# Optimization experiments

Hardware: AMD Instinct MI355X
Metric: run time of the kernel (lower is better)

Reference implementation:

```python
import jax, jax.numpy as jnp
import numpy as np

N = 16384   # nodes at current level
M = 8192    # nodes at next (coarser) level
E = 524288  # edges (avg degree 32)
D = 128     # in_feats == out_feats
LN_EPS = 1e-5


def setup_inputs() -> dict:
    key = jax.random.key(0)
    ks = jax.random.split(key, 10)
    curr_h = jax.random.normal(ks[0], (N, D), jnp.float32)
    next_h = jax.random.normal(ks[1], (M, D), jnp.float32)
    curr_inc = jax.random.uniform(ks[2], (N, M), jnp.float32)
    edge_src = jax.random.randint(ks[3], (E,), 0, N, jnp.int32)
    edge_dst = jax.random.randint(ks[4], (E,), 0, N, jnp.int32)
    Wc = jax.random.normal(ks[5], (D, D), jnp.float32) / np.float32(np.sqrt(D))
    Wf = jax.random.normal(ks[6], (D, D), jnp.float32) / np.float32(np.sqrt(D))
    bc = jnp.zeros((D,), jnp.float32)
    bf = jnp.zeros((D,), jnp.float32)
    conv_w = jax.random.uniform(ks[7], (D,), jnp.float32)
    topDown_w = jax.random.uniform(ks[8], (D,), jnp.float32)
    gamma = jnp.ones((D,), jnp.float32)
    beta = jnp.zeros((D,), jnp.float32)
    return dict(curr_h=curr_h, next_h=next_h, curr_inc=curr_inc,
                Wc=Wc, bc=bc, Wf=Wf, bf=bf, conv_w=conv_w,
                topDown_w=topDown_w, gamma=gamma, beta=beta,
                edge_src=edge_src, edge_dst=edge_dst)


def _graph_conv(x, W, b, src, dst, n):
    # DGL GraphConv, norm='both', on graph with self-loops added.
    ones = jnp.ones(src.shape[0], x.dtype)
    out_deg = jax.ops.segment_sum(ones, src, num_segments=n) + 1.0  # +1 self-loop
    in_deg = jax.ops.segment_sum(ones, dst, num_segments=n) + 1.0
    xn = x * jax.lax.rsqrt(out_deg)[:, None]
    # neighbor SpMM + self-loop contribution
    agg = jax.ops.segment_sum(xn[src], dst, num_segments=n) + xn
    agg = agg * jax.lax.rsqrt(in_deg)[:, None]
    return agg @ W + b


def reference(curr_h, next_h, curr_inc, Wc, bc, Wf, bf, conv_w,
              topDown_w, gamma, beta, edge_src, edge_dst):
    n = curr_h.shape[0]
    conv_layer = _graph_conv(curr_h, Wc, bc, edge_src, edge_dst, n) * conv_w[None, :]
    fused_in = curr_inc @ next_h  # dense incidence matmul [N, D]
    top_down = _graph_conv(fused_in, Wf, bf, edge_src, edge_dst, n) * topDown_w[None, :]
    res = (conv_layer + top_down) * 0.5  # update == 'MEAN' over stack of 2
    # LayerNorm over feature dim
    mu = jnp.mean(res, axis=-1, keepdims=True)
    var = jnp.mean(jnp.square(res - mu), axis=-1, keepdims=True)
    res = (res - mu) * jax.lax.rsqrt(var + LN_EPS) * gamma + beta
    res = jax.nn.relu(res)  # activation == 'RELU'
    # dropout: eval mode -> identity
    return res
```

## Files before the change

### kernel.cpp

```cpp
#include <hip/hip_runtime.h>

constexpr int Nn = 16384;
constexpr int Mm = 8192;
constexpr int Ee = 524288;
constexpr int Dd = 128;

typedef __attribute__((ext_vector_type(8))) short short8v;
typedef __attribute__((ext_vector_type(4))) short short4v;
typedef __attribute__((ext_vector_type(4))) float float4v;

static __device__ __forceinline__ short f2bf(float f) {
    unsigned u = __builtin_bit_cast(unsigned, f);
    u += 0x7fffu + ((u >> 16) & 1u);
    return (short)(u >> 16);
}

__global__ void k_zero_i(int* __restrict__ p, int n) {
    int i = blockIdx.x * 256 + threadIdx.x;
    if (i < n) p[i] = 0;
}

__global__ void k_deg_count(const int* __restrict__ src, const int* __restrict__ dst,
                            int* __restrict__ cnt_out, int* __restrict__ cnt_in) {
    int e = blockIdx.x * 256 + threadIdx.x;
    if (e < Ee) {
        atomicAdd(&cnt_out[src[e]], 1);
        atomicAdd(&cnt_in[dst[e]], 1);
    }
}

__global__ void k_deg_fin(const int* __restrict__ cnt_out, const int* __restrict__ cnt_in,
                          float* __restrict__ rs_out, float* __restrict__ rs_in) {
    int i = blockIdx.x * 256 + threadIdx.x;
    if (i < Nn) {
        rs_out[i] = rsqrtf((float)(cnt_out[i] + 1));
        rs_in[i]  = rsqrtf((float)(cnt_in[i] + 1));
    }
}

__global__ void k_scan(const int* __restrict__ cnt, int* __restrict__ row_start) {
    __shared__ int s[1024];
    int t = threadIdx.x;
    int base = t * 16;
    int local[16];
    int sum = 0;
#pragma unroll
    for (int i = 0; i < 16; i++) { local[i] = cnt[base + i]; sum += local[i]; }
    s[t] = sum;
    __syncthreads();
    for (int off = 1; off < 1024; off <<= 1) {
        int v = (t >= off) ? s[t - off] : 0;
        __syncthreads();
        s[t] += v;
        __syncthreads();
    }
    int run = s[t] - sum;
#pragma unroll
    for (int i = 0; i < 16; i++) { row_start[base + i] = run; run += local[i]; }
    if (t == 1023) row_start[16384] = s[1023];
}

__global__ void k_fill(const int* __restrict__ src, const int* __restrict__ dst,
                       const int* __restrict__ row_start, int* __restrict__ cursor,
                       int* __restrict__ ebuf) {
    int e = blockIdx.x * 256 + threadIdx.x;
    if (e < Ee) {
        int d = dst[e];
        int pos = atomicAdd(&cursor[d], 1);
        ebuf[row_start[d] + pos] = src[e];
    }
}

__global__ void k_prep(const float* __restrict__ Wc, const float* __restrict__ Wf,
                       const float* __restrict__ bc, const float* __restrict__ bf,
                       const float* __restrict__ cw, const float* __restrict__ tw,
                       float* __restrict__ Wp, float* __restrict__ bp) {
    int i = blockIdx.x * 256 + threadIdx.x;
    int r = i >> 7, j = i & 127;
    float w = (r < 128) ? Wc[r * 128 + j] * cw[j] : Wf[(r - 128) * 128 + j] * tw[j];
    Wp[i] = w;
    if (i < 128) bp[i] = bc[i] * cw[i] + bf[i] * tw[i];
}

__global__ void k_agg2(const float* __restrict__ x1, const float* __restrict__ x2,
                       const float* __restrict__ rs_o, const float* __restrict__ rs_i,
                       const int* __restrict__ row_start, const int* __restrict__ ebuf,
                       float* __restrict__ agg) {
    int d = blockIdx.x * 4 + (threadIdx.x >> 6);
    int lane = threadIdx.x & 63;
    int c = lane * 2;
    int beg = row_start[d], end = row_start[d + 1];
    float ax = 0.f, ay = 0.f, bx = 0.f, by = 0.f;
    int i = beg;
    for (; i + 1 < end; i += 2) {
        int s0 = ebuf[i], s1 = ebuf[i + 1];
        float r0 = rs_o[s0], r1 = rs_o[s1];
        float2 u0 = *(const float2*)(x1 + (size_t)s0 * 128 + c);
        float2 u1 = *(const float2*)(x1 + (size_t)s1 * 128 + c);
        float2 w0 = *(const float2*)(x2 + (size_t)s0 * 128 + c);
        float2 w1 = *(const float2*)(x2 + (size_t)s1 * 128 + c);
        ax += u0.x * r0 + u1.x * r1;
        ay += u0.y * r0 + u1.y * r1;
        bx += w0.x * r0 + w1.x * r1;
        by += w0.y * r0 + w1.y * r1;
    }
    if (i < end) {
        int s0 = ebuf[i];
        float r0 = rs_o[s0];
        float2 u0 = *(const float2*)(x1 + (size_t)s0 * 128 + c);
        float2 w0 = *(const float2*)(x2 + (size_t)s0 * 128 + c);
        ax += u0.x * r0;
        ay += u0.y * r0;
        bx += w0.x * r0;
        by += w0.y * r0;
    }
    float2 us = *(const float2*)(x1 + (size_t)d * 128 + c);
    float2 ws = *(const float2*)(x2 + (size_t)d * 128 + c);
    float ro = rs_o[d], ri = rs_i[d];
    float2 o1, o2;
    o1.x = (ax + us.x * ro) * ri;
    o1.y = (ay + us.y * ro) * ri;
    o2.x = (bx + ws.x * ro) * ri;
    o2.y = (by + ws.y * ro) * ri;
    *(float2*)(agg + (size_t)d * 256 + c) = o1;
    *(float2*)(agg + (size_t)d * 256 + 128 + c) = o2;
}

__global__ void k_bt(const float* __restrict__ B, short* __restrict__ Bt) {
    __shared__ short T[32][40];
    int kt = blockIdx.x & 255;
    int nt = blockIdx.x >> 8;
    int t = threadIdx.x;
    int r = t >> 3;
    int c4 = (t & 7) * 4;
    float4 v = *(const float4*)(B + (size_t)(kt * 32 + r) * 128 + nt * 32 + c4);
    T[c4 + 0][r] = f2bf(v.x);
    T[c4 + 1][r] = f2bf(v.y);
    T[c4 + 2][r] = f2bf(v.z);
    T[c4 + 3][r] = f2bf(v.w);
    __syncthreads();
    int nl = t >> 3, ks = (t & 7) * 4;
    *(short4v*)(Bt + (size_t)(nt * 32 + nl) * 8192 + kt * 32 + ks) =
        *(const short4v*)(&T[nl][ks]);
}

__launch_bounds__(256, 2)
__global__ void k_mfma_gemm(const float* __restrict__ A, const short* __restrict__ Bt,
                            float* __restrict__ C) {
    __shared__ short As[32 * 72];
    __shared__ short Bs[128 * 72];

    const int tid = threadIdx.x;
    const int lane = tid & 63;
    const int wv = tid >> 6;
    const int row0 = blockIdx.x * 32;

    const int ar = tid >> 3;
    const int ak = (tid & 7) * 8;
    const float* Ap = A + (size_t)(row0 + ar) * Mm + ak;

    const int bn = tid >> 1;
    const int bk = (tid & 1) * 32;
    const short* Bp = Bt + (size_t)bn * Mm + bk;

    const int fm = lane & 15;
    const int fk = (lane >> 4) * 8;

    float4v acc[2][2] = {};

    float4 a0A, a1A, a0B, a1B;
    short8v b0A, b1A, b2A, b3A, b0B, b1B, b2B, b3B;

#define LOADSET(s, koff)                                   \
    a0##s = *(const float4*)(Ap + (koff));                 \
    a1##s = *(const float4*)(Ap + (koff) + 4);             \
    b0##s = *(const short8v*)(Bp + (koff));                \
    b1##s = *(const short8v*)(Bp + (koff) + 8);            \
    b2##s = *(const short8v*)(Bp + (koff) + 16);           \
    b3##s = *(const short8v*)(Bp + (koff) + 24);

#define PHASE(s, knext)                                                        \
    {                                                                          \
        short8v ap;                                                            \
        ap[0] = f2bf(a0##s.x); ap[1] = f2bf(a0##s.y);                          \
        ap[2] = f2bf(a0##s.z); ap[3] = f2bf(a0##s.w);                          \
        ap[4] = f2bf(a1##s.x); ap[5] = f2bf(a1##s.y);                          \
        ap[6] = f2bf(a1##s.z); ap[7] = f2bf(a1##s.w);                          \
        __syncthreads();                      \
        *(short8v*)(&As[ar * 72 + ak]) = ap;                                   \
        *(short8v*)(&Bs[bn * 72 + bk +  0]) = b0##s;                           \
        *(short8v*)(&Bs[bn * 72 + bk +  8]) = b1##s;                           \
        *(short8v*)(&Bs[bn * 72 + bk + 16]) = b2##s;                           \
        *(short8v*)(&Bs[bn * 72 + bk + 24]) = b3##s;                           \
        __syncthreads();                                                       \
        if ((knext) < Mm) { LOADSET(s, knext) }                                \
        _Pragma("unroll")                                                      \
        for (int ks = 0; ks < 2; ks++) {                                       \
            const int kk = ks * 32 + fk;                                       \
            short8v a0f = *(const short8v*)(&As[fm * 72 + kk]);                \
            short8v a1f = *(const short8v*)(&As[(16 + fm) * 72 + kk]);         \
            short8v b0f = *(const short8v*)(&Bs[(wv * 32 + fm) * 72 + kk]);    \
            short8v b1f = *(const short8v*)(&Bs[(wv * 32 + 16 + fm) * 72 + kk]); \
            acc[0][0] = __builtin_amdgcn_mfma_f32_16x16x32_bf16(a0f, b0f, acc[0][0], 0, 0, 0); \
            acc[0][1] = __builtin_amdgcn_mfma_f32_16x16x32_bf16(a0f, b1f, acc[0][1], 0, 0, 0); \
            acc[1][0] = __builtin_amdgcn_mfma_f32_16x16x32_bf16(a1f, b0f, acc[1][0], 0, 0, 0); \
            acc[1][1] = __builtin_amdgcn_mfma_f32_16x16x32_bf16(a1f, b1f, acc[1][1], 0, 0, 0); \
        }                                                                      \
    }

    LOADSET(A, 0)
    LOADSET(B, 64)

    for (int k0 = 0; k0 < Mm; k0 += 128) {
        PHASE(A, k0 + 128)
        PHASE(B, k0 + 192)
    }
#undef PHASE
#undef LOADSET

    const int crow = (lane >> 4) * 4;
#pragma unroll
    for (int mt = 0; mt < 2; mt++)
#pragma unroll
        for (int nt = 0; nt < 2; nt++)
#pragma unroll
            for (int r = 0; r < 4; r++)
                C[(size_t)(row0 + mt * 16 + crow + r) * 128 + wv * 32 + nt * 16 + fm] =
                    acc[mt][nt][r];
}

__launch_bounds__(256, 2)
__global__ void k_gemm_ln(const float* __restrict__ A, const float* __restrict__ B,
                          const float* __restrict__ bias,
                          const float* __restrict__ gamma, const float* __restrict__ beta,
                          float* __restrict__ out) {
    __shared__ float As[32 * 36];
    __shared__ float Bs[32 * 128];

    const int tid = threadIdx.x;
    const int tx = tid & 31;
    const int ty = tid >> 5;
    const int c4 = tx * 4;
    const int r0 = ty * 4;
    const int row0 = blockIdx.x * 32;

    const int ar = tid >> 3;
    const int ak = (tid & 7) * 4;
    const float* Arow = A + (size_t)(row0 + ar) * 256 + ak;

    float acc[4][4] = {};

    for (int k0 = 0; k0 < 256; k0 += 32) {
        float4 av = *(const float4*)(Arow + k0);
        float4 bv[4];
#pragma unroll
        for (int t = 0; t < 4; t++) {
            int idx = tid + t * 256;
            int br = idx >> 5, bc = (idx & 31) * 4;
            bv[t] = *(const float4*)(B + (size_t)(k0 + br) * 128 + bc);
        }
        __syncthreads();
        As[(ak + 0) * 36 + ar] = av.x;
        As[(ak + 1) * 36 + ar] = av.y;
        As[(ak + 2) * 36 + ar] = av.z;
        As[(ak + 3) * 36 + ar] = av.w;
#pragma unroll
        for (int t = 0; t < 4; t++) {
            int idx = tid + t * 256;
            int br = idx >> 5, bc = (idx & 31) * 4;
            *(float4*)(Bs + br * 128 + bc) = bv[t];
        }
        __syncthreads();
#pragma unroll
        for (int kk = 0; kk < 32; kk++) {
            float4 a4 = *(const float4*)(As + kk * 36 + r0);
            float4 b4 = *(const float4*)(Bs + kk * 128 + c4);
            float a[4] = {a4.x, a4.y, a4.z, a4.w};
            float b[4] = {b4.x, b4.y, b4.z, b4.w};
#pragma unroll
            for (int i = 0; i < 4; i++)
#pragma unroll
                for (int j = 0; j < 4; j++)
                    acc[i][j] = fmaf(a[i], b[j], acc[i][j]);
        }
    }

    float4 bi = *(const float4*)(bias + c4);
    float4 g  = *(const float4*)(gamma + c4);
    float4 be = *(const float4*)(beta + c4);
#pragma unroll
    for (int i = 0; i < 4; i++) {
        float v0 = (acc[i][0] + bi.x) * 0.5f;
        float v1 = (acc[i][1] + bi.y) * 0.5f;
        float v2 = (acc[i][2] + bi.z) * 0.5f;
        float v3 = (acc[i][3] + bi.w) * 0.5f;
        float s1 = v0 + v1 + v2 + v3;
        float s2 = v0 * v0 + v1 * v1 + v2 * v2 + v3 * v3;
#pragma unroll
        for (int m = 16; m >= 1; m >>= 1) {
            s1 += __shfl_xor(s1, m);
            s2 += __shfl_xor(s2, m);
        }
        float mu  = s1 * (1.0f / 128.0f);
        float var = s2 * (1.0f / 128.0f) - mu * mu;
        float inv = rsqrtf(var + 1e-5f);
        float4 o;
        o.x = fmaxf((v0 - mu) * inv * g.x + be.x, 0.0f);
        o.y = fmaxf((v1 - mu) * inv * g.y + be.y, 0.0f);
        o.z = fmaxf((v2 - mu) * inv * g.z + be.z, 0.0f);
        o.w = fmaxf((v3 - mu) * inv * g.w + be.w, 0.0f);
        *(float4*)(out + (size_t)(row0 + r0 + i) * 128 + c4) = o;
    }
}

extern "C" void kernel_launch(void* const* d_in, const int* in_sizes, int n_in,
                              void* d_out, int out_size, void* d_ws, size_t ws_size,
                              hipStream_t stream) {
    const float* curr_h    = (const float*)d_in[0];
    const float* next_h    = (const float*)d_in[1];
    const float* curr_inc  = (const float*)d_in[2];
    const float* Wc        = (const float*)d_in[3];
    const float* bc        = (const float*)d_in[4];
    const float* Wf        = (const float*)d_in[5];
    const float* bf        = (const float*)d_in[6];
    const float* conv_w    = (const float*)d_in[7];
    const float* topDown_w = (const float*)d_in[8];
    const float* gamma     = (const float*)d_in[9];
    const float* beta      = (const float*)d_in[10];
    const int*   esrc      = (const int*)d_in[11];
    const int*   edst      = (const int*)d_in[12];
    float* out = (float*)d_out;

    char* w = (char*)d_ws;
    int*   cnt_out = (int*)w;    w += (size_t)Nn * 4;
    int*   cnt_in  = (int*)w;    w += (size_t)Nn * 4;
    int*   cursor  = (int*)w;    w += (size_t)Nn * 4;
    int*   row_st  = (int*)w;    w += (size_t)16388 * 4;
    int*   ebuf    = (int*)w;    w += (size_t)Ee * 4;
    float* rs_out  = (float*)w;  w += (size_t)Nn * 4;
    float* rs_in   = (float*)w;  w += (size_t)Nn * 4;
    short* Bt      = (short*)w;  w += (size_t)Dd * Mm * 2;
    float* fused   = (float*)w;  w += (size_t)Nn * Dd * 4;
    float* agg2    = (float*)w;  w += (size_t)Nn * 256 * 4;
    float* Wp      = (float*)w;  w += (size_t)256 * 128 * 4;
    float* bp      = (float*)w;  w += (size_t)1024;

    k_zero_i<<<(3 * Nn + 255) / 256, 256, 0, stream>>>(cnt_out, 3 * Nn);
    k_deg_count<<<Ee / 256, 256, 0, stream>>>(esrc, edst, cnt_out, cnt_in);
    k_deg_fin<<<Nn / 256, 256, 0, stream>>>(cnt_out, cnt_in, rs_out, rs_in);
    k_scan<<<1, 1024, 0, stream>>>(cnt_in, row_st);
    k_fill<<<Ee / 256, 256, 0, stream>>>(esrc, edst, row_st, cursor, ebuf);
    k_prep<<<128, 256, 0, stream>>>(Wc, Wf, bc, bf, conv_w, topDown_w, Wp, bp);

    k_bt<<<1024, 256, 0, stream>>>(next_h, Bt);
    k_mfma_gemm<<<Nn / 32, 256, 0, stream>>>(curr_inc, Bt, fused);

    k_agg2<<<Nn / 4, 256, 0, stream>>>(curr_h, fused, rs_out, rs_in, row_st, ebuf, agg2);
    k_gemm_ln<<<Nn / 32, 256, 0, stream>>>(agg2, Wp, bp, gamma, beta, out);
}
```

Baseline: 960.4 us.

## Apply dense projection before sparse aggregation and deepen GEMM prefetch pipeline

The order of graph aggregation and the linear layer is swapped. The combined [x1|x2]·Wp projection, scaled by rs_out, is now computed first into a 128-wide Z, so the SpMM gathers 128 floats per edge instead of 256, and LayerNorm is fused into the aggregation kernel. The big incidence GEMM also moves from two to four register prefetch stages and replaces __syncthreads with raw s_barrier plus explicit lgkmcnt waits and sched barriers, so global loads for the next stage can be issued before the barrier. The risks are higher register pressure in the GEMM and changed float summation order.

New measurement: 929.0 us. 3.3% less time.

```diff
diff --git a/kernel.cpp b/kernel.cpp
--- a/kernel.cpp
+++ b/kernel.cpp
@@ -80,50 +80,6 @@
     float w = (r < 128) ? Wc[r * 128 + j] * cw[j] : Wf[(r - 128) * 128 + j] * tw[j];
     Wp[i] = w;
     if (i < 128) bp[i] = bc[i] * cw[i] + bf[i] * tw[i];
-}
-
-__global__ void k_agg2(const float* __restrict__ x1, const float* __restrict__ x2,
-                       const float* __restrict__ rs_o, const float* __restrict__ rs_i,
-                       const int* __restrict__ row_start, const int* __restrict__ ebuf,
-                       float* __restrict__ agg) {
-    int d = blockIdx.x * 4 + (threadIdx.x >> 6);
-    int lane = threadIdx.x & 63;
-    int c = lane * 2;
-    int beg = row_start[d], end = row_start[d + 1];
-    float ax = 0.f, ay = 0.f, bx = 0.f, by = 0.f;
-    int i = beg;
-    for (; i + 1 < end; i += 2) {
-        int s0 = ebuf[i], s1 = ebuf[i + 1];
-        float r0 = rs_o[s0], r1 = rs_o[s1];
-        float2 u0 = *(const float2*)(x1 + (size_t)s0 * 128 + c);
-        float2 u1 = *(const float2*)(x1 + (size_t)s1 * 128 + c);
-        float2 w0 = *(const float2*)(x2 + (size_t)s0 * 128 + c);
-        float2 w1 = *(const float2*)(x2 + (size_t)s1 * 128 + c);
-        ax += u0.x * r0 + u1.x * r1;
-        ay += u0.y * r0 + u1.y * r1;
-        bx += w0.x * r0 + w1.x * r1;
-        by += w0.y * r0 + w1.y * r1;
-    }
-    if (i < end) {
-        int s0 = ebuf[i];
-        float r0 = rs_o[s0];
-        float2 u0 = *(const float2*)(x1 + (size_t)s0 * 128 + c);
-        float2 w0 = *(const float2*)(x2 + (size_t)s0 * 128 + c);
-        ax += u0.x * r0;
-        ay += u0.y * r0;
-        bx += w0.x * r0;
-        by += w0.y * r0;
-    }
-    float2 us = *(const float2*)(x1 + (size_t)d * 128 + c);
-    float2 ws = *(const float2*)(x2 + (size_t)d * 128 + c);
-    float ro = rs_o[d], ri = rs_i[d];
-    float2 o1, o2;
-    o1.x = (ax + us.x * ro) * ri;
-    o1.y = (ay + us.y * ro) * ri;
-    o2.x = (bx + ws.x * ro) * ri;
-    o2.y = (by + ws.y * ro) * ri;
-    *(float2*)(agg + (size_t)d * 256 + c) = o1;
-    *(float2*)(agg + (size_t)d * 256 + 128 + c) = o2;
 }
 
 __global__ void k_bt(const float* __restrict__ B, short* __restrict__ Bt) {
@@ -168,8 +124,9 @@
 
     float4v acc[2][2] = {};
 
-    float4 a0A, a1A, a0B, a1B;
+    float4 a0A, a1A, a0B, a1B, a0C, a1C, a0D, a1D;
     short8v b0A, b1A, b2A, b3A, b0B, b1B, b2B, b3B;
+    short8v b0C, b1C, b2C, b3C, b0D, b1D, b2D, b3D;
 
 #define LOADSET(s, koff)                                   \
     a0##s = *(const float4*)(Ap + (koff));                 \
@@ -186,14 +143,19 @@
         ap[2] = f2bf(a0##s.z); ap[3] = f2bf(a0##s.w);                          \
         ap[4] = f2bf(a1##s.x); ap[5] = f2bf(a1##s.y);                          \
         ap[6] = f2bf(a1##s.z); ap[7] = f2bf(a1##s.w);                          \
-        __syncthreads();                      \
+        __builtin_amdgcn_sched_barrier(0);                                     \
+        __builtin_amdgcn_s_barrier();          \
+        __builtin_amdgcn_sched_barrier(0);                                     \
         *(short8v*)(&As[ar * 72 + ak]) = ap;                                   \
         *(short8v*)(&Bs[bn * 72 + bk +  0]) = b0##s;                           \
         *(short8v*)(&Bs[bn * 72 + bk +  8]) = b1##s;                           \
         *(short8v*)(&Bs[bn * 72 + bk + 16]) = b2##s;                           \
         *(short8v*)(&Bs[bn * 72 + bk + 24]) = b3##s;                           \
-        __syncthreads();                                                       \
-        if ((knext) < Mm) { LOADSET(s, knext) }                                \
+        if ((knext) < Mm) { LOADSET(s, knext) }   \
+        asm volatile("s_waitcnt lgkmcnt(0)" ::: "memory");                     \
+        __builtin_amdgcn_sched_barrier(0);                                     \
+        __builtin_amdgcn_s_barrier();                 \
+        __builtin_amdgcn_sched_barrier(0);                                     \
         _Pragma("unroll")                                                      \
         for (int ks = 0; ks < 2; ks++) {                                       \
             const int kk = ks * 32 + fk;                                       \
@@ -210,10 +172,14 @@
 
     LOADSET(A, 0)
     LOADSET(B, 64)
-
-    for (int k0 = 0; k0 < Mm; k0 += 128) {
-        PHASE(A, k0 + 128)
-        PHASE(B, k0 + 192)
+    LOADSET(C, 128)
+    LOADSET(D, 192)
+
+    for (int k0 = 0; k0 < Mm; k0 += 256) {
+        PHASE(A, k0 + 256)
+        PHASE(B, k0 + 320)
+        PHASE(C, k0 + 384)
+        PHASE(D, k0 + 448)
     }
 #undef PHASE
 #undef LOADSET
@@ -230,10 +196,9 @@
 }
 
 __launch_bounds__(256, 2)
-__global__ void k_gemm_ln(const float* __restrict__ A, const float* __restrict__ B,
-                          const float* __restrict__ bias,
-                          const float* __restrict__ gamma, const float* __restrict__ beta,
-                          float* __restrict__ out) {
+__global__ void k_gemmZ(const float* __restrict__ x1, const float* __restrict__ x2,
+                        const float* __restrict__ B, const float* __restrict__ rs_o,
+                        float* __restrict__ Zs) {
     __shared__ float As[32 * 36];
     __shared__ float Bs[32 * 128];
 
@@ -246,12 +211,14 @@
 
     const int ar = tid >> 3;
     const int ak = (tid & 7) * 4;
-    const float* Arow = A + (size_t)(row0 + ar) * 256 + ak;
 
     float acc[4][4] = {};
 
     for (int k0 = 0; k0 < 256; k0 += 32) {
-        float4 av = *(const float4*)(Arow + k0);
+        const float* src = (k0 < 128)
+            ? x1 + (size_t)(row0 + ar) * 128 + k0 + ak
+            : x2 + (size_t)(row0 + ar) * 128 + (k0 - 128) + ak;
+        float4 av = *(const float4*)src;
         float4 bv[4];
 #pragma unroll
         for (int t = 0; t < 4; t++) {
@@ -285,32 +252,61 @@
         }
     }
 
-    float4 bi = *(const float4*)(bias + c4);
-    float4 g  = *(const float4*)(gamma + c4);
-    float4 be = *(const float4*)(beta + c4);
 #pragma unroll
     for (int i = 0; i < 4; i++) {
-        float v0 = (acc[i][0] + bi.x) * 0.5f;
-        float v1 = (acc[i][1] + bi.y) * 0.5f;
-        float v2 = (acc[i][2] + bi.z) * 0.5f;
-        float v3 = (acc[i][3] + bi.w) * 0.5f;
-        float s1 = v0 + v1 + v2 + v3;
-        float s2 = v0 * v0 + v1 * v1 + v2 * v2 + v3 * v3;
-#pragma unroll
-        for (int m = 16; m >= 1; m >>= 1) {
-            s1 += __shfl_xor(s1, m);
-            s2 += __shfl_xor(s2, m);
-        }
-        float mu  = s1 * (1.0f / 128.0f);
-        float var = s2 * (1.0f / 128.0f) - mu * mu;
-        float inv = rsqrtf(var + 1e-5f);
-        float4 o;
-        o.x = fmaxf((v0 - mu) * inv * g.x + be.x, 0.0f);
-        o.y = fmaxf((v1 - mu) * inv * g.y + be.y, 0.0f);
-        o.z = fmaxf((v2 - mu) * inv * g.z + be.z, 0.0f);
-        o.w = fmaxf((v3 - mu) * inv * g.w + be.w, 0.0f);
-        *(float4*)(out + (size_t)(row0 + r0 + i) * 128 + c4) = o;
-    }
+        float ro = rs_o[row0 + r0 + i];
+        float4 v = {acc[i][0] * ro, acc[i][1] * ro, acc[i][2] * ro, acc[i][3] * ro};
+        *(float4*)(Zs + (size_t)(row0 + r0 + i) * 128 + c4) = v;
+    }
+}
+
+__global__ void k_aggln(const float* __restrict__ Zs, const float* __restrict__ rs_i,
+                        const int* __restrict__ row_start, const int* __restrict__ ebuf,
+                        const float* __restrict__ bp, const float* __restrict__ gamma,
+                        const float* __restrict__ beta, float* __restrict__ out) {
+    int d = blockIdx.x * 4 + (threadIdx.x >> 6);
+    int lane = threadIdx.x & 63;
+    int c = lane * 2;
+    int beg = row_start[d], end = row_start[d + 1];
+    float ax = 0.f, ay = 0.f;
+    int i = beg;
+    for (; i + 3 < end; i += 4) {
+        int s0 = ebuf[i], s1 = ebuf[i + 1], s2 = ebuf[i + 2], s3 = ebuf[i + 3];
+        float2 v0 = *(const float2*)(Zs + (size_t)s0 * 128 + c);
+        float2 v1 = *(const float2*)(Zs + (size_t)s1 * 128 + c);
+        float2 v2 = *(const float2*)(Zs + (size_t)s2 * 128 + c);
+        float2 v3 = *(const float2*)(Zs + (size_t)s3 * 128 + c);
+        ax += (v0.x + v1.x) + (v2.x + v3.x);
+        ay += (v0.y + v1.y) + (v2.y + v3.y);
+    }
+    for (; i < end; ++i) {
+        int s0 = ebuf[i];
+        float2 v0 = *(const float2*)(Zs + (size_t)s0 * 128 + c);
+        ax += v0.x;
+        ay += v0.y;
+    }
+    float2 self = *(const float2*)(Zs + (size_t)d * 128 + c);
+    float ri = rs_i[d];
+    float2 bpv = *(const float2*)(bp + c);
+    float vx = (ri * (ax + self.x) + bpv.x) * 0.5f;
+    float vy = (ri * (ay + self.y) + bpv.y) * 0.5f;
+
+    float s1 = vx + vy;
+    float s2 = vx * vx + vy * vy;
+#pragma unroll
+    for (int m = 32; m >= 1; m >>= 1) {
+        s1 += __shfl_xor(s1, m);
+        s2 += __shfl_xor(s2, m);
+    }
+    float mu  = s1 * (1.0f / 128.0f);
+    float var = s2 * (1.0f / 128.0f) - mu * mu;
+    float inv = rsqrtf(var + 1e-5f);
+    float2 g = *(const float2*)(gamma + c);
+    float2 b = *(const float2*)(beta + c);
+    float2 o;
+    o.x = fmaxf((vx - mu) * inv * g.x + b.x, 0.0f);
+    o.y = fmaxf((vy - mu) * inv * g.y + b.y, 0.0f);
+    *(float2*)(out + (size_t)d * 128 + c) = o;
 }
 
 extern "C" void kernel_launch(void* const* d_in, const int* in_sizes, int n_in,
@@ -341,7 +337,7 @@
     float* rs_in   = (float*)w;  w += (size_t)Nn * 4;
     short* Bt      = (short*)w;  w += (size_t)Dd * Mm * 2;
     float* fused   = (float*)w;  w += (size_t)Nn * Dd * 4;
-    float* agg2    = (float*)w;  w += (size_t)Nn * 256 * 4;
+    float* Zs      = (float*)w;  w += (size_t)Nn * Dd * 4;
     float* Wp      = (float*)w;  w += (size_t)256 * 128 * 4;
     float* bp      = (float*)w;  w += (size_t)1024;
 
@@ -355,6 +351,6 @@
     k_bt<<<1024, 256, 0, stream>>>(next_h, Bt);
     k_mfma_gemm<<<Nn / 32, 256, 0, stream>>>(curr_inc, Bt, fused);
 
-    k_agg2<<<Nn / 4, 256, 0, stream>>>(curr_h, fused, rs_out, rs_in, row_st, ebuf, agg2);
-    k_gemm_ln<<<Nn / 32, 256, 0, stream>>>(agg2, Wp, bp, gamma, beta, out);
-}
+    k_gemmZ<<<Nn / 32, 256, 0, stream>>>(curr_h, fused, Wp, rs_out, Zs);
+    k_aggln<<<Nn / 4, 256, 0, stream>>>(Zs, rs_in, row_st, ebuf, bp, gamma, beta, out);
+}
```
